# Optimization experiments

Hardware: AMD Instinct MI355X
Metric: run time of the kernel (lower is better)

Reference implementation:

```python
import jax, jax.numpy as jnp
import numpy as np

B, T, C, H = 2, 2048, 1024, 16
D = C // H  # head dim, even
NEG = -1e10  # masked_fill value used by the torch module (not -inf)


def _rope_cache(dim, max_positions):
    # Faithful to source: theta_i = 1/10000**(-2*(i-1)/dim), i = arange(dim//2)
    i = jnp.arange(dim // 2, dtype=jnp.float32)
    theta = 1.0 / (10000.0 ** (-2.0 * (i - 1.0) / dim))
    ang = jnp.arange(max_positions, dtype=jnp.float32)[:, None] * theta[None, :]  # [T, D/2]
    return jnp.cos(ang), jnp.sin(ang)


def _apply_rope(x, cos, sin):
    # x: [B,H,T,D]; consecutive pairs form complex numbers (x[...,2j], x[...,2j+1])
    xp = x.reshape(*x.shape[:-1], D // 2, 2)
    xr, xi = xp[..., 0], xp[..., 1]
    rr = xr * cos - xi * sin
    ri = xr * sin + xi * cos
    return jnp.stack([rr, ri], axis=-1).reshape(x.shape)


def setup_inputs() -> dict:
    key = jax.random.key(0)
    ks = jax.random.split(key, 5)
    s = 1.0 / np.sqrt(C)
    return {
        'x': jax.random.normal(ks[0], (B, T, C), jnp.float32),
        'Wq': jax.random.normal(ks[1], (C, C), jnp.float32) * s,
        'bq': jnp.zeros((C,), jnp.float32),
        'Wk': jax.random.normal(ks[2], (C, C), jnp.float32) * s,
        'bk': jnp.zeros((C,), jnp.float32),
        'Wv': jax.random.normal(ks[3], (C, C), jnp.float32) * s,
        'bv': jnp.zeros((C,), jnp.float32),
        'Wp': jax.random.normal(ks[4], (C, C), jnp.float32) * s,
        'bp': jnp.zeros((C,), jnp.float32),
    }


def reference(x, Wq, bq, Wk, bk, Wv, bv, Wp, bp):
    cos, sin = _rope_cache(D, T)  # [T, D/2]
    def split_heads(h):
        return h.reshape(B, T, H, D).transpose(0, 2, 1, 3)  # [B,H,T,D]
    q = split_heads(x @ Wq.T + bq)
    k = split_heads(x @ Wk.T + bk)
    v = split_heads(x @ Wv.T + bv)
    q = _apply_rope(q, cos, sin)
    k = _apply_rope(k, cos, sin)
    att = jnp.einsum('bhqd,bhkd->bhqk', q, k) * (1.0 / np.sqrt(D))  # [B,H,T,T]
    causal = jnp.tril(jnp.ones((T, T), bool))
    att = jnp.where(causal, att, NEG)
    att = jax.nn.softmax(att, axis=-1)
    y = jnp.einsum('bhqk,bhkd->bhqd', att, v)
    y = y.transpose(0, 2, 1, 3).reshape(B, T, C)
    return y @ Wp.T + bp
```

## Files before the change

kernel.cpp:

```cpp
#include <hip/hip_runtime.h>

#define SEQ 2048
#define CDIM 1024
#define NHEAD 16
#define HDIM 64

typedef __bf16 bf16x8 __attribute__((ext_vector_type(8)));
typedef __bf16 bf16x4v __attribute__((ext_vector_type(4)));
typedef float f32x4 __attribute__((ext_vector_type(4)));

typedef const __attribute__((address_space(1))) char* gcp_t;
typedef __attribute__((address_space(3))) char* lcp_t;

__device__ __forceinline__ void gload16(const void* g, void* l) {
    __builtin_amdgcn_global_load_lds((gcp_t)g, (lcp_t)l, 16, 0, 0);
}

__device__ __forceinline__ unsigned short f2bf(float f) {
    unsigned int u = __float_as_uint(f);
    u += 0x7fffu + ((u >> 16) & 1u);
    return (unsigned short)(u >> 16);
}


__global__ void cvt_kernel(const float* __restrict__ src, unsigned short* __restrict__ dst, int n4) {
    int i = blockIdx.x * blockDim.x + threadIdx.x;
    if (i < n4) {
        float4 v = ((const float4*)src)[i];
        ushort4 o;
        o.x = f2bf(v.x); o.y = f2bf(v.y); o.z = f2bf(v.z); o.w = f2bf(v.w);
        ((ushort4*)dst)[i] = o;
    }
}

__global__ void cvtw_kernel(const float* __restrict__ Wq, const float* __restrict__ Wk,
                            const float* __restrict__ Wv, const float* __restrict__ Wp,
                            unsigned short* __restrict__ wqkv, unsigned short* __restrict__ wpb) {
    int i = blockIdx.x * blockDim.x + threadIdx.x;
    int which = i >> 18, r = i & 262143;
    const float* s = (which == 0) ? Wq : (which == 1) ? Wk : (which == 2) ? Wv : Wp;
    unsigned short* d = (which < 3) ? (wqkv + (size_t)which * 1048576) : wpb;
    float4 v = ((const float4*)s)[r];
    ushort4 o;
    o.x = f2bf(v.x); o.y = f2bf(v.y); o.z = f2bf(v.z); o.w = f2bf(v.w);
    ((ushort4*)d)[r] = o;
}

__global__ void rope_kernel(float2* __restrict__ cstab) {
    int idx = blockIdx.x * blockDim.x + threadIdx.x;
    int j = idx & 31, t = idx >> 5;
    float e = -2.0f * ((float)j - 1.0f) / 64.0f;
    float denom = (float)pow(10000.0, (double)e);
    float theta = 1.0f / denom;
    float ang = (float)t * theta;
    cstab[idx] = make_float2(cosf(ang), sinf(ang));
}

template <int MODE>
__global__ __launch_bounds__(256) void gemm_bt(
    const unsigned short* __restrict__ A, const unsigned short* __restrict__ Bm,
    const float* __restrict__ b0, const float* __restrict__ b1, const float* __restrict__ b2,
    unsigned short* __restrict__ qb, unsigned short* __restrict__ kb,
    unsigned short* __restrict__ vtb, float* __restrict__ outf,
    const float2* __restrict__ cstab)
{
    constexpr int K = 1024;
    constexpr int NIT = K / 32;
    __shared__ __align__(16) unsigned short As[2][128 * 32];
    __shared__ __align__(16) unsigned short Bs[2][128 * 32];
    const int tid = threadIdx.x, lane = tid & 63, wid = tid >> 6;
    const int m0 = blockIdx.y * 128, n0 = blockIdx.x * 128;
    const int wr = wid >> 1, wc = wid & 1;

    f32x4 acc[4][4] = {};

    const char* Ag = (const char*)(A + (size_t)m0 * K);
    const char* Bg = (const char*)(Bm + (size_t)n0 * K);
    const int r0 = tid >> 2, cb = (tid & 3) * 16;
    const int r1 = r0 + 64;
    const int ldsw = wid << 10;

    auto stage = [&](int k0, int bufi) {
        gload16(Ag + (size_t)r0 * 2048 + k0 * 2 + cb, (char*)As[bufi] + ldsw);
        gload16(Ag + (size_t)r1 * 2048 + k0 * 2 + cb, (char*)As[bufi] + 4096 + ldsw);
        gload16(Bg + (size_t)r0 * 2048 + k0 * 2 + cb, (char*)Bs[bufi] + ldsw);
        gload16(Bg + (size_t)r1 * 2048 + k0 * 2 + cb, (char*)Bs[bufi] + 4096 + ldsw);
    };

    stage(0, 0);
    __syncthreads();

    for (int it = 0; it < NIT; ++it) {
        const int cur = it & 1;
        if (it + 1 < NIT) stage((it + 1) * 32, cur ^ 1);
        bf16x8 af[4], bfr[4];
#pragma unroll
        for (int am = 0; am < 4; ++am)
            af[am] = *(const bf16x8*)(As[cur] + (wr * 64 + am * 16 + (lane & 15)) * 32 + (lane >> 4) * 8);
#pragma unroll
        for (int an = 0; an < 4; ++an)
            bfr[an] = *(const bf16x8*)(Bs[cur] + (wc * 64 + an * 16 + (lane & 15)) * 32 + (lane >> 4) * 8);
#pragma unroll
        for (int am = 0; am < 4; ++am)
#pragma unroll
            for (int an = 0; an < 4; ++an)
                acc[am][an] = __builtin_amdgcn_mfma_f32_16x16x32_bf16(af[am], bfr[an], acc[am][an], 0, 0, 0);
        __syncthreads();
    }

    if (MODE == 0) {
        const float QSCL = 0.18033688011112042f;
#pragma unroll
        for (int an = 0; an < 4; ++an) {
            const int ng = n0 + wc * 64 + an * 16 + (lane & 15);
            const int which = ng >> 10, nl = ng & 1023;
            const int h = nl >> 6, d = nl & 63;
            const float* bptr = (which == 0) ? b0 : (which == 1) ? b1 : b2;
            const float bias = bptr[nl];
            if (which < 2) {
                unsigned short* dst = (which == 0) ? qb : kb;
                const float qs = (which == 0) ? QSCL : 1.0f;
                const int j = d >> 1;
#pragma unroll
                for (int am = 0; am < 4; ++am) {
#pragma unroll
                    for (int i = 0; i < 4; ++i) {
                        const int row = m0 + wr * 64 + am * 16 + (lane >> 4) * 4 + i;
                        const int bb = row >> 11, t = row & 2047;
                        float v = acc[am][an][i] + bias;
                        float p = __shfl_xor(v, 1);
                        const float2 cs = cstab[t * 32 + j];
                        v = (d & 1) ? fmaf(v, cs.x, p * cs.y) : fmaf(v, cs.x, -p * cs.y);
                        dst[((size_t)((bb * 16 + h) * 2048 + t)) * 64 + d] = f2bf(v * qs);
                    }
                }
            } else {
#pragma unroll
                for (int am = 0; am < 4; ++am) {
                    const int rowb = m0 + wr * 64 + am * 16 + (lane >> 4) * 4;
                    const int bb = rowb >> 11, t = rowb & 2047;
                    ushort4 pk;
                    pk.x = f2bf(acc[am][an][0] + bias);
                    pk.y = f2bf(acc[am][an][1] + bias);
                    pk.z = f2bf(acc[am][an][2] + bias);
                    pk.w = f2bf(acc[am][an][3] + bias);
                    *(ushort4*)(vtb + ((size_t)((bb * 16 + h) * 64 + d)) * 2048 + t) = pk;
                }
            }
        }
    } else {
#pragma unroll
        for (int an = 0; an < 4; ++an) {
            const int col = n0 + wc * 64 + an * 16 + (lane & 15);
            const float bias = b0[col];
#pragma unroll
            for (int am = 0; am < 4; ++am)
#pragma unroll
                for (int i = 0; i < 4; ++i) {
                    const int row = m0 + wr * 64 + am * 16 + (lane >> 4) * 4 + i;
                    outf[(size_t)row * 1024 + col] = acc[am][an][i] + bias;
                }
        }
    }
}

__global__ __launch_bounds__(256) void attn_kernel(
    const unsigned short* __restrict__ qb, const unsigned short* __restrict__ kb,
    const unsigned short* __restrict__ vtb, unsigned short* __restrict__ yb)
{
    __shared__ __align__(16) unsigned short Ks[2][64 * 64];
    __shared__ __align__(16) unsigned short Vs[2][64 * 64];
    __shared__ __align__(16) unsigned short Ps[4][16 * 64];
    const int tid = threadIdx.x, lane = tid & 63, wid = tid >> 6;
    const int bh = blockIdx.y;
    const int b = bh >> 4, h = bh & 15;
    const int qt = (bh & 16) ? (31 - blockIdx.x) : blockIdx.x;
    const int q0 = qt * 64;
    const int qw = q0 + wid * 16;
    const unsigned short* Qg = qb + (size_t)bh * SEQ * HDIM;
    const char* Kg = (const char*)(kb + (size_t)bh * SEQ * HDIM);
    const char* Vg = (const char*)(vtb + (size_t)bh * HDIM * SEQ);

    bf16x8 qf[2];
#pragma unroll
    for (int kf = 0; kf < 2; ++kf)
        qf[kf] = *(const bf16x8*)(Qg + (size_t)(qw + (lane & 15)) * 64 + kf * 32 + (lane >> 4) * 8);

    f32x4 o[4] = {};
    float mrun = -3e38f;
    float lrun = 0.0f;

    const int nt = qt + 1;
    const int cr0 = tid >> 3, cc0 = ((tid & 7) * 16) ^ ((cr0 & 7) << 4);
    const int cr1 = cr0 + 32, cc1 = ((tid & 7) * 16) ^ ((cr1 & 7) << 4);
    const int ldsw = wid << 10;

    auto stage = [&](int kt, int bufi) {
        const size_t kv0 = (size_t)kt * 64;
        gload16(Kg + (kv0 + cr0) * 128 + cc0, (char*)Ks[bufi] + ldsw);
        gload16(Kg + (kv0 + cr1) * 128 + cc1, (char*)Ks[bufi] + 4096 + ldsw);
        gload16(Vg + (size_t)cr0 * 4096 + kv0 * 2 + cc0, (char*)Vs[bufi] + ldsw);
        gload16(Vg + (size_t)cr1 * 4096 + kv0 * 2 + cc1, (char*)Vs[bufi] + 4096 + ldsw);
    };

    stage(0, 0);
    __syncthreads();

    for (int kt = 0; kt < nt; ++kt) {
        const int cur = kt & 1;
        if (kt + 1 < nt) stage(kt + 1, cur ^ 1);
        const int kv0 = kt * 64;
        {
            f32x4 s[4] = {};
            __builtin_amdgcn_s_setprio(1);
#pragma unroll
            for (int kf = 0; kf < 2; ++kf) {
                bf16x8 kfr[4];
#pragma unroll
                for (int an = 0; an < 4; ++an) {
                    const int r = an * 16 + (lane & 15);
                    kfr[an] = *(const bf16x8*)((const char*)Ks[cur] + r * 128 + ((kf * 64 + (lane >> 4) * 16) ^ ((r & 7) << 4)));
                }
#pragma unroll
                for (int an = 0; an < 4; ++an)
                    s[an] = __builtin_amdgcn_mfma_f32_16x16x32_bf16(kfr[an], qf[kf], s[an], 0, 0, 0);
            }
            __builtin_amdgcn_s_setprio(0);
            const bool need_mask = (kv0 + 63 > qw);
            const int qg = qw + (lane & 15);
            const int kbase = kv0 + ((lane >> 4) << 2);
            float p[4][4];
            float mx = -3e38f;
#pragma unroll
            for (int an = 0; an < 4; ++an)
#pragma unroll
                for (int i = 0; i < 4; ++i) {
                    float v = s[an][i];
                    if (need_mask && (kbase + an * 16 + i > qg)) v = -3e38f;
                    p[an][i] = v;
                    mx = fmaxf(mx, v);
                }
            mx = fmaxf(mx, __shfl_xor(mx, 16));
            mx = fmaxf(mx, __shfl_xor(mx, 32));
            if (!__all(mx <= mrun + 8.0f)) {
                const float mnew = fmaxf(mrun, mx);
                const float fsc = __builtin_amdgcn_exp2f(mrun - mnew);
                lrun *= fsc;
#pragma unroll
                for (int dn = 0; dn < 4; ++dn) o[dn] *= fsc;
                mrun = mnew;
            }
            float rs = 0.0f;
#pragma unroll
            for (int an = 0; an < 4; ++an)
#pragma unroll
                for (int i = 0; i < 4; ++i) {
                    p[an][i] = __builtin_amdgcn_exp2f(p[an][i] - mrun);
                    rs += p[an][i];
                }
            rs += __shfl_xor(rs, 16);
            rs += __shfl_xor(rs, 32);
            lrun += rs;
            const int ql = lane & 15;
            char* pb = (char*)Ps[wid] + ql * 128;
            const int xr = (ql & 7) << 4;
            const int gb = (lane >> 4) << 3;
#pragma unroll
            for (int an = 0; an < 4; ++an) {
                bf16x4v pk;
                pk[0] = (__bf16)p[an][0]; pk[1] = (__bf16)p[an][1];
                pk[2] = (__bf16)p[an][2]; pk[3] = (__bf16)p[an][3];
                *(bf16x4v*)(pb + ((an * 32 + gb) ^ xr)) = pk;
            }
            __builtin_amdgcn_s_setprio(1);
#pragma unroll
            for (int kf = 0; kf < 2; ++kf) {
                bf16x8 vf[4], pf;
#pragma unroll
                for (int dn = 0; dn < 4; ++dn) {
                    const int r = dn * 16 + (lane & 15);
                    vf[dn] = *(const bf16x8*)((const char*)Vs[cur] + r * 128 + ((kf * 64 + (lane >> 4) * 16) ^ ((r & 7) << 4)));
                }
                {
                    const int qlr = lane & 15;
                    pf = *(const bf16x8*)((const char*)Ps[wid] + qlr * 128 + ((kf * 64 + (lane >> 4) * 16) ^ ((qlr & 7) << 4)));
                }
#pragma unroll
                for (int dn = 0; dn < 4; ++dn)
                    o[dn] = __builtin_amdgcn_mfma_f32_16x16x32_bf16(vf[dn], pf, o[dn], 0, 0, 0);
            }
            __builtin_amdgcn_s_setprio(0);
        }
        __syncthreads();
    }

    {
        const float inv = 1.0f / lrun;
        const int qg = qw + (lane & 15);
        unsigned short* yrow = yb + (size_t)(b * SEQ + qg) * CDIM + h * 64;
#pragma unroll
        for (int dn = 0; dn < 4; ++dn) {
            const int d = dn * 16 + ((lane >> 4) << 2);
            bf16x4v pk;
            pk[0] = (__bf16)(o[dn][0] * inv);
            pk[1] = (__bf16)(o[dn][1] * inv);
            pk[2] = (__bf16)(o[dn][2] * inv);
            pk[3] = (__bf16)(o[dn][3] * inv);
            *(bf16x4v*)(yrow + d) = pk;
        }
    }
}


extern "C" void kernel_launch(void* const* d_in, const int* in_sizes, int n_in,
                              void* d_out, int out_size, void* d_ws, size_t ws_size,
                              hipStream_t stream) {
    (void)in_sizes; (void)n_in; (void)out_size; (void)ws_size;
    const float* x  = (const float*)d_in[0];
    const float* Wq = (const float*)d_in[1];
    const float* bq = (const float*)d_in[2];
    const float* Wk = (const float*)d_in[3];
    const float* bk = (const float*)d_in[4];
    const float* Wv = (const float*)d_in[5];
    const float* bv = (const float*)d_in[6];
    const float* Wp = (const float*)d_in[7];
    const float* bp = (const float*)d_in[8];
    float* out = (float*)d_out;

    char* ws = (char*)d_ws;
    size_t off = 0;
    auto take = [&](size_t bytes) -> char* {
        char* p = ws + off;
        off = (off + bytes + 255) & ~(size_t)255;
        return p;
    };
    float2* cstab = (float2*)take((size_t)SEQ * 32 * 8);
    unsigned short* xb   = (unsigned short*)take((size_t)4096 * 1024 * 2);
    unsigned short* wqkv = (unsigned short*)take((size_t)3 * 1024 * 1024 * 2);
    unsigned short* wpb  = (unsigned short*)take((size_t)1024 * 1024 * 2);
    unsigned short* qbuf = (unsigned short*)take((size_t)32 * SEQ * HDIM * 2);
    unsigned short* kbuf = (unsigned short*)take((size_t)32 * SEQ * HDIM * 2);
    unsigned short* vtb  = (unsigned short*)take((size_t)32 * HDIM * SEQ * 2);
    unsigned short* yb   = (unsigned short*)take((size_t)4096 * 1024 * 2);

    rope_kernel<<<256, 256, 0, stream>>>(cstab);
    cvt_kernel<<<4096, 256, 0, stream>>>(x, xb, 1048576);
    cvtw_kernel<<<4096, 256, 0, stream>>>(Wq, Wk, Wv, Wp, wqkv, wpb);

    dim3 g0(24, 32);
    gemm_bt<0><<<g0, 256, 0, stream>>>(xb, wqkv, bq, bk, bv, qbuf, kbuf, vtb, nullptr, cstab);
    dim3 g1(32, 32);
    attn_kernel<<<g1, 256, 0, stream>>>(qbuf, kbuf, vtb, yb);
    dim3 g2(8, 32);
    gemm_bt<1><<<g2, 256, 0, stream>>>(yb, wpb, bp, nullptr, nullptr, nullptr, nullptr, nullptr, out, cstab);
}
```

Baseline: 139.5 us.

## Split causal attention KV range across blocks with flash-decoding style combine

Each query tile's causal key range is split into 1-4 chunks depending on the tile's depth, giving 80 slots per head. Each chunk writes unnormalized partial outputs plus running max and sum, and a new combine kernel merges them with log-sum-exp weights. This balances per-block work across the triangular causal workload and raises block count from 1024 to 2560. The cost is an extra kernel launch, partial outputs stored in bf16 before merging, and extra global memory traffic.

```diff
diff --git a/kernel.cpp b/kernel.cpp
--- a/kernel.cpp
+++ b/kernel.cpp
@@ -4,6 +4,7 @@
 #define CDIM 1024
 #define NHEAD 16
 #define HDIM 64
+#define NSLOT 80
 
 typedef __bf16 bf16x8 __attribute__((ext_vector_type(8)));
 typedef __bf16 bf16x4v __attribute__((ext_vector_type(4)));
@@ -21,6 +22,9 @@
     u += 0x7fffu + ((u >> 16) & 1u);
     return (unsigned short)(u >> 16);
 }
+
+__device__ __forceinline__ float bflo(unsigned int u) { return __uint_as_float(u << 16); }
+__device__ __forceinline__ float bfhi(unsigned int u) { return __uint_as_float(u & 0xffff0000u); }
 
 
 __global__ void cvt_kernel(const float* __restrict__ src, unsigned short* __restrict__ dst, int n4) {
@@ -166,15 +170,22 @@
 
 __global__ __launch_bounds__(256) void attn_kernel(
     const unsigned short* __restrict__ qb, const unsigned short* __restrict__ kb,
-    const unsigned short* __restrict__ vtb, unsigned short* __restrict__ yb)
+    const unsigned short* __restrict__ vtb, unsigned short* __restrict__ pb,
+    float2* __restrict__ ml)
 {
     __shared__ __align__(16) unsigned short Ks[2][64 * 64];
     __shared__ __align__(16) unsigned short Vs[2][64 * 64];
     __shared__ __align__(16) unsigned short Ps[4][16 * 64];
     const int tid = threadIdx.x, lane = tid & 63, wid = tid >> 6;
-    const int bh = blockIdx.y;
-    const int b = bh >> 4, h = bh & 15;
-    const int qt = (bh & 16) ? (31 - blockIdx.x) : blockIdx.x;
+    const int bh = blockIdx.x;
+    const int y = blockIdx.y;
+    int qt, ck, nc;
+    if (y < 32)      { qt = 31 - (y >> 2); ck = y & 3; nc = 4; }
+    else if (y < 56) { int t2 = y - 32; int k3 = t2 / 3; qt = 23 - k3; ck = t2 - k3 * 3; nc = 3; }
+    else if (y < 72) { int t2 = y - 56; qt = 15 - (t2 >> 1); ck = t2 & 1; nc = 2; }
+    else             { qt = 7 - (y - 72); ck = 0; nc = 1; }
+    const int nt = qt + 1;
+    const int t0 = ck * nt / nc, t1 = (ck + 1) * nt / nc;
     const int q0 = qt * 64;
     const int qw = q0 + wid * 16;
     const unsigned short* Qg = qb + (size_t)bh * SEQ * HDIM;
@@ -190,7 +201,6 @@
     float mrun = -3e38f;
     float lrun = 0.0f;
 
-    const int nt = qt + 1;
     const int cr0 = tid >> 3, cc0 = ((tid & 7) * 16) ^ ((cr0 & 7) << 4);
     const int cr1 = cr0 + 32, cc1 = ((tid & 7) * 16) ^ ((cr1 & 7) << 4);
     const int ldsw = wid << 10;
@@ -203,12 +213,12 @@
         gload16(Vg + (size_t)cr1 * 4096 + kv0 * 2 + cc1, (char*)Vs[bufi] + 4096 + ldsw);
     };
 
-    stage(0, 0);
+    stage(t0, 0);
     __syncthreads();
 
-    for (int kt = 0; kt < nt; ++kt) {
-        const int cur = kt & 1;
-        if (kt + 1 < nt) stage(kt + 1, cur ^ 1);
+    for (int kt = t0; kt < t1; ++kt) {
+        const int cur = (kt - t0) & 1;
+        if (kt + 1 < t1) stage(kt + 1, cur ^ 1);
         const int kv0 = kt * 64;
         {
             f32x4 s[4] = {};
@@ -262,7 +272,7 @@
             rs += __shfl_xor(rs, 32);
             lrun += rs;
             const int ql = lane & 15;
-            char* pb = (char*)Ps[wid] + ql * 128;
+            char* pbs = (char*)Ps[wid] + ql * 128;
             const int xr = (ql & 7) << 4;
             const int gb = (lane >> 4) << 3;
 #pragma unroll
@@ -270,7 +280,7 @@
                 bf16x4v pk;
                 pk[0] = (__bf16)p[an][0]; pk[1] = (__bf16)p[an][1];
                 pk[2] = (__bf16)p[an][2]; pk[3] = (__bf16)p[an][3];
-                *(bf16x4v*)(pb + ((an * 32 + gb) ^ xr)) = pk;
+                *(bf16x4v*)(pbs + ((an * 32 + gb) ^ xr)) = pk;
             }
             __builtin_amdgcn_s_setprio(1);
 #pragma unroll
@@ -295,20 +305,80 @@
     }
 
     {
-        const float inv = 1.0f / lrun;
-        const int qg = qw + (lane & 15);
-        unsigned short* yrow = yb + (size_t)(b * SEQ + qg) * CDIM + h * 64;
+        const size_t sbase = (size_t)bh * NSLOT + y;
+        const int qloc = wid * 16 + (lane & 15);
+        unsigned short* prow = pb + (sbase * 64 + qloc) * 64;
 #pragma unroll
         for (int dn = 0; dn < 4; ++dn) {
             const int d = dn * 16 + ((lane >> 4) << 2);
             bf16x4v pk;
-            pk[0] = (__bf16)(o[dn][0] * inv);
-            pk[1] = (__bf16)(o[dn][1] * inv);
-            pk[2] = (__bf16)(o[dn][2] * inv);
-            pk[3] = (__bf16)(o[dn][3] * inv);
-            *(bf16x4v*)(yrow + d) = pk;
-        }
+            pk[0] = (__bf16)o[dn][0];
+            pk[1] = (__bf16)o[dn][1];
+            pk[2] = (__bf16)o[dn][2];
+            pk[3] = (__bf16)o[dn][3];
+            *(bf16x4v*)(prow + d) = pk;
+        }
+        if ((lane >> 4) == 0) ml[sbase * 64 + qloc] = make_float2(mrun, lrun);
     }
+}
+
+__global__ __launch_bounds__(256) void combine_kernel(
+    const unsigned short* __restrict__ pb, const float2* __restrict__ ml,
+    unsigned short* __restrict__ yb)
+{
+    const int qt = blockIdx.x, bh = blockIdx.y;
+    const int b = bh >> 4, h = bh & 15;
+    int base, nc;
+    if (qt >= 24)      { base = (31 - qt) * 4;      nc = 4; }
+    else if (qt >= 16) { base = 32 + (23 - qt) * 3; nc = 3; }
+    else if (qt >= 8)  { base = 56 + (15 - qt) * 2; nc = 2; }
+    else               { base = 72 + (7 - qt);      nc = 1; }
+    const int t = threadIdx.x;
+    const int q = t >> 2;
+    const int d0 = (t & 3) * 16;
+    const size_t sbase = (size_t)bh * NSLOT + base;
+
+    float m[4], l[4];
+    float M = -3e38f;
+#pragma unroll
+    for (int c = 0; c < 4; ++c)
+        if (c < nc) {
+            float2 v = ml[(sbase + c) * 64 + q];
+            m[c] = v.x; l[c] = v.y;
+            M = fmaxf(M, v.x);
+        }
+    float L = 0.0f;
+    float w[4];
+#pragma unroll
+    for (int c = 0; c < 4; ++c)
+        if (c < nc) {
+            w[c] = __builtin_amdgcn_exp2f(m[c] - M);
+            L += l[c] * w[c];
+        }
+    const float invL = 1.0f / L;
+
+    float acc[16] = {};
+#pragma unroll
+    for (int c = 0; c < 4; ++c)
+        if (c < nc) {
+            const float wc = w[c] * invL;
+            const uint4* src = (const uint4*)(pb + ((sbase + c) * 64 + q) * 64 + d0);
+            uint4 A = src[0], B = src[1];
+            const unsigned int ua[8] = {A.x, A.y, A.z, A.w, B.x, B.y, B.z, B.w};
+#pragma unroll
+            for (int k = 0; k < 8; ++k) {
+                acc[2 * k]     = fmaf(wc, bflo(ua[k]), acc[2 * k]);
+                acc[2 * k + 1] = fmaf(wc, bfhi(ua[k]), acc[2 * k + 1]);
+            }
+        }
+
+    unsigned int outw[8];
+#pragma unroll
+    for (int k = 0; k < 8; ++k)
+        outw[k] = (unsigned int)f2bf(acc[2 * k]) | ((unsigned int)f2bf(acc[2 * k + 1]) << 16);
+    uint4* dst = (uint4*)(yb + (size_t)(b * SEQ + qt * 64 + q) * CDIM + h * 64 + d0);
+    dst[0] = make_uint4(outw[0], outw[1], outw[2], outw[3]);
+    dst[1] = make_uint4(outw[4], outw[5], outw[6], outw[7]);
 }
 
 
@@ -342,6 +412,8 @@
     unsigned short* kbuf = (unsigned short*)take((size_t)32 * SEQ * HDIM * 2);
     unsigned short* vtb  = (unsigned short*)take((size_t)32 * HDIM * SEQ * 2);
     unsigned short* yb   = (unsigned short*)take((size_t)4096 * 1024 * 2);
+    unsigned short* pbuf = (unsigned short*)take((size_t)32 * NSLOT * 64 * 64 * 2);
+    float2* mlb          = (float2*)take((size_t)32 * NSLOT * 64 * 8);
 
     rope_kernel<<<256, 256, 0, stream>>>(cstab);
     cvt_kernel<<<4096, 256, 0, stream>>>(x, xb, 1048576);
@@ -349,8 +421,10 @@
 
     dim3 g0(24, 32);
     gemm_bt<0><<<g0, 256, 0, stream>>>(xb, wqkv, bq, bk, bv, qbuf, kbuf, vtb, nullptr, cstab);
-    dim3 g1(32, 32);
-    attn_kernel<<<g1, 256, 0, stream>>>(qbuf, kbuf, vtb, yb);
+    dim3 g1(32, NSLOT);
+    attn_kernel<<<g1, 256, 0, stream>>>(qbuf, kbuf, vtb, pbuf, mlb);
+    dim3 gc(32, 32);
+    combine_kernel<<<gc, 256, 0, stream>>>(pbuf, mlb, yb);
     dim3 g2(8, 32);
     gemm_bt<1><<<g2, 256, 0, stream>>>(yb, wpb, bp, nullptr, nullptr, nullptr, nullptr, nullptr, out, cstab);
 }
```

Measured after the change: 140.5 us. No clear change (+0.7%).

## Use 256x256-tile QKV GEMM with swizzled LDS and smaller-tile output projection

Applied to the files above, without the earlier changes.

Replaces the 128x128 QKV projection GEMM with a dedicated 512-thread kernel using 256x256 tiles, a 64-wide K step, XOR-swizzled LDS layout, grouped block ordering for L2 reuse, and loads interleaved with MFMA phases. The output projection GEMM gets XOR-swizzled LDS and switches to 64-row tiles, doubling its grid to fill more CUs. Aims to raise MFMA utilisation and cut LDS bank conflicts. It uses more LDS and registers per block, and the QKV grid of 192 blocks may underfill the GPU.

```diff
diff --git a/kernel.cpp b/kernel.cpp
--- a/kernel.cpp
+++ b/kernel.cpp
@@ -21,6 +21,8 @@
     u += 0x7fffu + ((u >> 16) & 1u);
     return (unsigned short)(u >> 16);
 }
+
+__device__ __forceinline__ int swz16(int r) { return ((r >> 1) & 3) << 4; }
 
 
 __global__ void cvt_kernel(const float* __restrict__ src, unsigned short* __restrict__ dst, int n4) {
@@ -56,35 +58,159 @@
     cstab[idx] = make_float2(cosf(ang), sinf(ang));
 }
 
-template <int MODE>
-__global__ __launch_bounds__(256) void gemm_bt(
+__global__ __launch_bounds__(512, 1) void gemm_qkv256(
     const unsigned short* __restrict__ A, const unsigned short* __restrict__ Bm,
     const float* __restrict__ b0, const float* __restrict__ b1, const float* __restrict__ b2,
     unsigned short* __restrict__ qb, unsigned short* __restrict__ kb,
-    unsigned short* __restrict__ vtb, float* __restrict__ outf,
-    const float2* __restrict__ cstab)
+    unsigned short* __restrict__ vtb, const float2* __restrict__ cstab)
+{
+    constexpr int NT = 16;
+    constexpr int NXT = 12, CPX = 24;
+    __shared__ __align__(16) char As[2][256 * 128];
+    __shared__ __align__(16) char Bs[2][256 * 128];
+    const int tid = threadIdx.x, lane = tid & 63, wid = tid >> 6;
+    const int wr = wid >> 2, wc = wid & 3;
+    const int bid = blockIdx.x;
+    const int swz = (bid & 7) * CPX + (bid >> 3);
+    const int mt = swz / NXT;
+    const int m0 = mt * 256, n0 = (swz - mt * NXT) * 256;
+
+    f32x4 acc[8][4] = {};
+
+    const char* Ag = (const char*)A + (size_t)m0 * 2048;
+    const char* Bg = (const char*)Bm + (size_t)n0 * 2048;
+    const int r0 = tid >> 3, cb = (tid & 7) * 16;
+
+    auto stageA = [&](int k0, int bufi, int s) {
+        const int r = r0 + 64 * s;
+        gload16(Ag + (size_t)r * 2048 + k0 * 2 + (cb ^ ((r & 7) << 4)),
+                As[bufi] + s * 8192 + wid * 1024);
+    };
+    auto stageB = [&](int k0, int bufi, int s) {
+        const int r = r0 + 64 * s;
+        gload16(Bg + (size_t)r * 2048 + k0 * 2 + (cb ^ ((r & 7) << 4)),
+                Bs[bufi] + s * 8192 + wid * 1024);
+    };
+
+#pragma unroll
+    for (int s = 0; s < 4; ++s) { stageA(0, 0, s); stageB(0, 0, s); }
+    asm volatile("s_waitcnt vmcnt(0)" ::: "memory");
+    __builtin_amdgcn_s_barrier();
+
+    for (int t = 0; t < NT; ++t) {
+        const int cur = t & 1;
+        const char* Ac = As[cur];
+        const char* Bc = Bs[cur];
+        const int k1 = (t + 1) * 64;
+        bf16x8 bfr[4][2];
+#pragma unroll
+        for (int p = 0; p < 4; ++p) {
+            if (p == 0) {
+#pragma unroll
+                for (int fc = 0; fc < 4; ++fc)
+#pragma unroll
+                    for (int kf = 0; kf < 2; ++kf) {
+                        const int r = wc * 64 + fc * 16 + (lane & 15);
+                        bfr[fc][kf] = *(const bf16x8*)(Bc + r * 128 + ((kf * 64 + (lane >> 4) * 16) ^ ((r & 7) << 4)));
+                    }
+            }
+            bf16x8 af[2][2];
+#pragma unroll
+            for (int fa = 0; fa < 2; ++fa)
+#pragma unroll
+                for (int kf = 0; kf < 2; ++kf) {
+                    const int r = wr * 128 + (p * 2 + fa) * 16 + (lane & 15);
+                    af[fa][kf] = *(const bf16x8*)(Ac + r * 128 + ((kf * 64 + (lane >> 4) * 16) ^ ((r & 7) << 4)));
+                }
+            if (t + 1 < NT) { stageA(k1, cur ^ 1, p); stageB(k1, cur ^ 1, p); }
+            __builtin_amdgcn_s_barrier();
+            __builtin_amdgcn_s_setprio(1);
+#pragma unroll
+            for (int kf = 0; kf < 2; ++kf)
+#pragma unroll
+                for (int fa = 0; fa < 2; ++fa)
+#pragma unroll
+                    for (int fc = 0; fc < 4; ++fc)
+                        acc[p * 2 + fa][fc] = __builtin_amdgcn_mfma_f32_16x16x32_bf16(
+                            af[fa][kf], bfr[fc][kf], acc[p * 2 + fa][fc], 0, 0, 0);
+            __builtin_amdgcn_s_setprio(0);
+        }
+        asm volatile("s_waitcnt vmcnt(0)" ::: "memory");
+        __builtin_amdgcn_s_barrier();
+    }
+
+    const float QSCL = 0.18033688011112042f;
+#pragma unroll
+    for (int fc = 0; fc < 4; ++fc) {
+        const int ng = n0 + wc * 64 + fc * 16 + (lane & 15);
+        const int which = ng >> 10, nl = ng & 1023;
+        const int h = nl >> 6, d = nl & 63;
+        const float* bptr = (which == 0) ? b0 : (which == 1) ? b1 : b2;
+        const float bias = bptr[nl];
+        if (which < 2) {
+            unsigned short* dst = (which == 0) ? qb : kb;
+            const float qs = (which == 0) ? QSCL : 1.0f;
+            const int j = d >> 1;
+#pragma unroll
+            for (int fr = 0; fr < 8; ++fr) {
+#pragma unroll
+                for (int i = 0; i < 4; ++i) {
+                    const int row = m0 + wr * 128 + fr * 16 + (lane >> 4) * 4 + i;
+                    const int bb = row >> 11, tt = row & 2047;
+                    float v = acc[fr][fc][i] + bias;
+                    float pp = __shfl_xor(v, 1);
+                    const float2 cs = cstab[tt * 32 + j];
+                    v = (d & 1) ? fmaf(v, cs.x, pp * cs.y) : fmaf(v, cs.x, -pp * cs.y);
+                    dst[((size_t)((bb * 16 + h) * 2048 + tt)) * 64 + d] = f2bf(v * qs);
+                }
+            }
+        } else {
+#pragma unroll
+            for (int fr = 0; fr < 8; ++fr) {
+                const int rowb = m0 + wr * 128 + fr * 16 + (lane >> 4) * 4;
+                const int bb = rowb >> 11, tt = rowb & 2047;
+                ushort4 pk;
+                pk.x = f2bf(acc[fr][fc][0] + bias);
+                pk.y = f2bf(acc[fr][fc][1] + bias);
+                pk.z = f2bf(acc[fr][fc][2] + bias);
+                pk.w = f2bf(acc[fr][fc][3] + bias);
+                *(ushort4*)(vtb + ((size_t)((bb * 16 + h) * 64 + d)) * 2048 + tt) = pk;
+            }
+        }
+    }
+}
+
+template <int MODE, int BM>
+__global__ __launch_bounds__(256) void gemm_bt(
+    const unsigned short* __restrict__ A, const unsigned short* __restrict__ Bm,
+    const float* __restrict__ b0,
+    float* __restrict__ outf)
 {
     constexpr int K = 1024;
     constexpr int NIT = K / 32;
-    __shared__ __align__(16) unsigned short As[2][128 * 32];
-    __shared__ __align__(16) unsigned short Bs[2][128 * 32];
+    constexpr int NR = (BM == 128) ? 4 : 2;
+    __shared__ __align__(16) char As[2][BM * 64];
+    __shared__ __align__(16) char Bs[2][128 * 64];
     const int tid = threadIdx.x, lane = tid & 63, wid = tid >> 6;
-    const int m0 = blockIdx.y * 128, n0 = blockIdx.x * 128;
-    const int wr = wid >> 1, wc = wid & 1;
-
-    f32x4 acc[4][4] = {};
+    const int m0 = blockIdx.y * BM, n0 = blockIdx.x * 128;
+    const int wr = (BM == 128) ? ((wid >> 1) * 64) : 0;
+    const int wc = (BM == 128) ? ((wid & 1) * 64) : (wid * 32);
+
+    f32x4 acc[4][NR] = {};
 
     const char* Ag = (const char*)(A + (size_t)m0 * K);
     const char* Bg = (const char*)(Bm + (size_t)n0 * K);
     const int r0 = tid >> 2, cb = (tid & 3) * 16;
-    const int r1 = r0 + 64;
     const int ldsw = wid << 10;
 
     auto stage = [&](int k0, int bufi) {
-        gload16(Ag + (size_t)r0 * 2048 + k0 * 2 + cb, (char*)As[bufi] + ldsw);
-        gload16(Ag + (size_t)r1 * 2048 + k0 * 2 + cb, (char*)As[bufi] + 4096 + ldsw);
-        gload16(Bg + (size_t)r0 * 2048 + k0 * 2 + cb, (char*)Bs[bufi] + ldsw);
-        gload16(Bg + (size_t)r1 * 2048 + k0 * 2 + cb, (char*)Bs[bufi] + 4096 + ldsw);
+        char* Ad = As[bufi];
+        char* Bd = Bs[bufi];
+        gload16(Ag + (size_t)r0 * 2048 + k0 * 2 + (cb ^ swz16(r0)), Ad + ldsw);
+        if constexpr (BM == 128)
+            gload16(Ag + (size_t)(r0 + 64) * 2048 + k0 * 2 + (cb ^ swz16(r0 + 64)), Ad + 4096 + ldsw);
+        gload16(Bg + (size_t)r0 * 2048 + k0 * 2 + (cb ^ swz16(r0)), Bd + ldsw);
+        gload16(Bg + (size_t)(r0 + 64) * 2048 + k0 * 2 + (cb ^ swz16(r0 + 64)), Bd + 4096 + ldsw);
     };
 
     stage(0, 0);
@@ -93,74 +219,39 @@
     for (int it = 0; it < NIT; ++it) {
         const int cur = it & 1;
         if (it + 1 < NIT) stage((it + 1) * 32, cur ^ 1);
-        bf16x8 af[4], bfr[4];
+        const char* Ac = As[cur];
+        const char* Bc = Bs[cur];
+        const int fs = (lane >> 4) * 16;
+        bf16x8 af[4], bfr[NR];
+#pragma unroll
+        for (int am = 0; am < 4; ++am) {
+            const int r = wr + am * 16 + (lane & 15);
+            af[am] = *(const bf16x8*)(Ac + r * 64 + (fs ^ swz16(r)));
+        }
+#pragma unroll
+        for (int an = 0; an < NR; ++an) {
+            const int r = wc + an * 16 + (lane & 15);
+            bfr[an] = *(const bf16x8*)(Bc + r * 64 + (fs ^ swz16(r)));
+        }
 #pragma unroll
         for (int am = 0; am < 4; ++am)
-            af[am] = *(const bf16x8*)(As[cur] + (wr * 64 + am * 16 + (lane & 15)) * 32 + (lane >> 4) * 8);
-#pragma unroll
-        for (int an = 0; an < 4; ++an)
-            bfr[an] = *(const bf16x8*)(Bs[cur] + (wc * 64 + an * 16 + (lane & 15)) * 32 + (lane >> 4) * 8);
-#pragma unroll
-        for (int am = 0; am < 4; ++am)
-#pragma unroll
-            for (int an = 0; an < 4; ++an)
+#pragma unroll
+            for (int an = 0; an < NR; ++an)
                 acc[am][an] = __builtin_amdgcn_mfma_f32_16x16x32_bf16(af[am], bfr[an], acc[am][an], 0, 0, 0);
         __syncthreads();
     }
 
-    if (MODE == 0) {
-        const float QSCL = 0.18033688011112042f;
-#pragma unroll
-        for (int an = 0; an < 4; ++an) {
-            const int ng = n0 + wc * 64 + an * 16 + (lane & 15);
-            const int which = ng >> 10, nl = ng & 1023;
-            const int h = nl >> 6, d = nl & 63;
-            const float* bptr = (which == 0) ? b0 : (which == 1) ? b1 : b2;
-            const float bias = bptr[nl];
-            if (which < 2) {
-                unsigned short* dst = (which == 0) ? qb : kb;
-                const float qs = (which == 0) ? QSCL : 1.0f;
-                const int j = d >> 1;
-#pragma unroll
-                for (int am = 0; am < 4; ++am) {
-#pragma unroll
-                    for (int i = 0; i < 4; ++i) {
-                        const int row = m0 + wr * 64 + am * 16 + (lane >> 4) * 4 + i;
-                        const int bb = row >> 11, t = row & 2047;
-                        float v = acc[am][an][i] + bias;
-                        float p = __shfl_xor(v, 1);
-                        const float2 cs = cstab[t * 32 + j];
-                        v = (d & 1) ? fmaf(v, cs.x, p * cs.y) : fmaf(v, cs.x, -p * cs.y);
-                        dst[((size_t)((bb * 16 + h) * 2048 + t)) * 64 + d] = f2bf(v * qs);
-                    }
-                }
-            } else {
-#pragma unroll
-                for (int am = 0; am < 4; ++am) {
-                    const int rowb = m0 + wr * 64 + am * 16 + (lane >> 4) * 4;
-                    const int bb = rowb >> 11, t = rowb & 2047;
-                    ushort4 pk;
-                    pk.x = f2bf(acc[am][an][0] + bias);
-                    pk.y = f2bf(acc[am][an][1] + bias);
-                    pk.z = f2bf(acc[am][an][2] + bias);
-                    pk.w = f2bf(acc[am][an][3] + bias);
-                    *(ushort4*)(vtb + ((size_t)((bb * 16 + h) * 64 + d)) * 2048 + t) = pk;
-                }
-            }
-        }
-    } else {
-#pragma unroll
-        for (int an = 0; an < 4; ++an) {
-            const int col = n0 + wc * 64 + an * 16 + (lane & 15);
-            const float bias = b0[col];
-#pragma unroll
-            for (int am = 0; am < 4; ++am)
-#pragma unroll
-                for (int i = 0; i < 4; ++i) {
-                    const int row = m0 + wr * 64 + am * 16 + (lane >> 4) * 4 + i;
-                    outf[(size_t)row * 1024 + col] = acc[am][an][i] + bias;
-                }
-        }
+#pragma unroll
+    for (int an = 0; an < NR; ++an) {
+        const int col = n0 + wc + an * 16 + (lane & 15);
+        const float bias = b0[col];
+#pragma unroll
+        for (int am = 0; am < 4; ++am)
+#pragma unroll
+            for (int i = 0; i < 4; ++i) {
+                const int row = m0 + wr + am * 16 + (lane >> 4) * 4 + i;
+                outf[(size_t)row * 1024 + col] = acc[am][an][i] + bias;
+            }
     }
 }
 
@@ -262,7 +353,7 @@
             rs += __shfl_xor(rs, 32);
             lrun += rs;
             const int ql = lane & 15;
-            char* pb = (char*)Ps[wid] + ql * 128;
+            char* pbs = (char*)Ps[wid] + ql * 128;
             const int xr = (ql & 7) << 4;
             const int gb = (lane >> 4) << 3;
 #pragma unroll
@@ -270,7 +361,7 @@
                 bf16x4v pk;
                 pk[0] = (__bf16)p[an][0]; pk[1] = (__bf16)p[an][1];
                 pk[2] = (__bf16)p[an][2]; pk[3] = (__bf16)p[an][3];
-                *(bf16x4v*)(pb + ((an * 32 + gb) ^ xr)) = pk;
+                *(bf16x4v*)(pbs + ((an * 32 + gb) ^ xr)) = pk;
             }
             __builtin_amdgcn_s_setprio(1);
 #pragma unroll
@@ -347,10 +438,9 @@
     cvt_kernel<<<4096, 256, 0, stream>>>(x, xb, 1048576);
     cvtw_kernel<<<4096, 256, 0, stream>>>(Wq, Wk, Wv, Wp, wqkv, wpb);
 
-    dim3 g0(24, 32);
-    gemm_bt<0><<<g0, 256, 0, stream>>>(xb, wqkv, bq, bk, bv, qbuf, kbuf, vtb, nullptr, cstab);
+    gemm_qkv256<<<192, 512, 0, stream>>>(xb, wqkv, bq, bk, bv, qbuf, kbuf, vtb, cstab);
     dim3 g1(32, 32);
     attn_kernel<<<g1, 256, 0, stream>>>(qbuf, kbuf, vtb, yb);
-    dim3 g2(8, 32);
-    gemm_bt<1><<<g2, 256, 0, stream>>>(yb, wpb, bp, nullptr, nullptr, nullptr, nullptr, nullptr, out, cstab);
-}
+    dim3 g2(8, 64);
+    gemm_bt<1, 64><<<g2, 256, 0, stream>>>(yb, wpb, bp, out);
+}
```

Measured after the change: 134.2 us. 1.04x faster.
